# Kernel tuning notes

Measured on AMD Instinct MI355X. Metric: run time of the kernel, lower is better.

Reference implementation:

```python
import jax, jax.numpy as jnp
import numpy as np

GRID_SIZE = 5
SPLINE_ORDER = 3
N_COEF = GRID_SIZE + SPLINE_ORDER  # 8
NUM_NODES = 100000
NUM_EDGES = 1200000
NUM_GRAPHS = 512
D = 64
N_TARGETS = 10


def _grid():
    # uniform grid on [-1, 1] extended by spline_order knots on each side (efficient-kan default)
    h = 2.0 / GRID_SIZE
    return jnp.arange(-SPLINE_ORDER, GRID_SIZE + SPLINE_ORDER + 1, dtype=jnp.float32) * h - 1.0


def b_splines(x):
    # x: (N, in) -> (N, in, N_COEF) via Cox-de Boor recursion
    g = _grid()
    xe = x[..., None]
    bases = ((xe >= g[:-1]) & (xe < g[1:])).astype(x.dtype)
    for k in range(1, SPLINE_ORDER + 1):
        left = (xe - g[: -(k + 1)]) / (g[k:-1] - g[: -(k + 1)])
        right = (g[k + 1:] - xe) / (g[k + 1:] - g[1:-k])
        bases = left * bases[..., :-1] + right * bases[..., 1:]
    return bases


def kan_linear(x, base_w, spline_w, scaler):
    # efficient-kan KANLinear: silu base branch + standalone-scaled spline branch
    base = jax.nn.silu(x) @ base_w.T
    sb = b_splines(x)  # (N, in, N_COEF)
    spline = jnp.einsum('nig,oig->no', sb, spline_w * scaler[..., None])
    return base + spline


def setup_inputs() -> dict:
    key = jax.random.key(0)
    ks = jax.random.split(key, 12)
    inp = {
        'x': jax.random.normal(ks[0], (NUM_NODES, D), dtype=jnp.float32),
        'edge_index': jax.random.randint(ks[1], (2, NUM_EDGES), 0, NUM_NODES, dtype=jnp.int64),
        'batch': jnp.sort(jax.random.randint(ks[2], (NUM_NODES,), 0, NUM_GRAPHS, dtype=jnp.int64)),
        # GINConv layer 0 KAN (D -> D)
        'base_w0': jax.random.normal(ks[3], (D, D), dtype=jnp.float32) * 0.1,
        'spline_w0': jax.random.normal(ks[4], (D, D, N_COEF), dtype=jnp.float32) * 0.1,
        'scaler0': jax.random.normal(ks[5], (D, D), dtype=jnp.float32) * 0.1 + 1.0,
        # GINConv layer 1 KAN (D -> D)
        'base_w1': jax.random.normal(ks[6], (D, D), dtype=jnp.float32) * 0.1,
        'spline_w1': jax.random.normal(ks[7], (D, D, N_COEF), dtype=jnp.float32) * 0.1,
        'scaler1': jax.random.normal(ks[8], (D, D), dtype=jnp.float32) * 0.1 + 1.0,
        # head KAN (D -> N_TARGETS)
        'base_wh': jax.random.normal(ks[9], (N_TARGETS, D), dtype=jnp.float32) * 0.1,
        'spline_wh': jax.random.normal(ks[10], (N_TARGETS, D, N_COEF), dtype=jnp.float32) * 0.1,
        'scaler_h': jax.random.normal(ks[11], (N_TARGETS, D), dtype=jnp.float32) * 0.1 + 1.0,
    }
    return inp


def reference(x, edge_index, batch, base_w0, spline_w0, scaler0,
              base_w1, spline_w1, scaler1, base_wh, spline_wh, scaler_h):
    src, dst = edge_index[0], edge_index[1]
    n = x.shape[0]
    # GINConv layer 0: nn((1+eps)*x + sum_{j in N(i)} x_j), eps=0; dropout is eval-mode identity
    agg = jax.ops.segment_sum(x[src], dst, num_segments=n)
    h = kan_linear(x + agg, base_w0, spline_w0, scaler0)
    # GINConv layer 1
    agg = jax.ops.segment_sum(h[src], dst, num_segments=n)
    h = kan_linear(h + agg, base_w1, spline_w1, scaler1)
    # global_add_pool over graphs, then KAN head
    pooled = jax.ops.segment_sum(h, batch, num_segments=NUM_GRAPHS)
    return kan_linear(pooled, base_wh, spline_wh, scaler_h)
```

## Files before the change

kernel.cpp:

```cpp
#include <hip/hip_runtime.h>
#include <hip/hip_fp16.h>
#include <math.h>

#define NODES   100000
#define EDGES   1200000
#define GRAPHS  512
#define DIM     64
#define NT      10
#define KTOT    576

#define NB      512
#define NBUSED  391
#define EPB     4096
#define CAP     4608

#define KSTAGE     96
#define WTL_STRIDE 104
#define V_STRIDE   72

#define S3B     ((EDGES + EPB - 1) / EPB)
#define PREPB   ((2 * DIM * KTOT) / 512)
#define CONVB   ((NODES * 16 + 32 + 511) / 512)

typedef _Float16 f16x8  __attribute__((ext_vector_type(8)));
typedef __fp16   fp16x2 __attribute__((ext_vector_type(2)));
typedef __attribute__((ext_vector_type(4))) float frag_cd;

__device__ __forceinline__ float silu(float x) {
    return x / (1.f + __expf(-x));
}

__device__ __forceinline__ unsigned packh2(float a, float b) {
    fp16x2 h = __builtin_amdgcn_cvt_pkrtz(a, b);
    return __builtin_bit_cast(unsigned, h);
}

__device__ __forceinline__ void acc_h8(float* a, uint4 p) {
    union { uint4 u; __half2 h[4]; } up; up.u = p;
#pragma unroll
    for (int j = 0; j < 4; ++j) {
        float2 f = __half22float2(up.h[j]);
        a[2 * j]     += f.x;
        a[2 * j + 1] += f.y;
    }
}

__device__ __forceinline__ f16x8 bases_frag(float xv) {
    float tt  = fmaf(xv, 2.5f, 5.5f);
    float fm  = floorf(tt);
    int   m   = (int)fm;
    float u   = tt - fm;
    float um1 = 1.f - u;
    float v3  = u * u * u * (1.f / 6.f);
    float v0  = um1 * um1 * um1 * (1.f / 6.f);
    float B2m1 = 0.5f * ((u + 1.f) * um1 + (2.f - u) * u);
    float v1  = ((u + 2.f) * um1 * um1 * 0.5f + (2.f - u) * B2m1) * (1.f / 3.f);
    float v2  = ((u + 1.f) * B2m1 + (3.f - u) * u * u * 0.5f) * (1.f / 3.f);

    unsigned d0 = packh2(v0, v1);
    unsigned d1 = packh2(v2, v3);
    int p = m - 3;
    int B = p >> 1;
    bool odd = (p & 1) != 0;
    unsigned e1 = __builtin_amdgcn_alignbit(d1, d0, 16);
    unsigned W0 = odd ? (d0 << 16) : d0;
    unsigned W1 = odd ? e1 : d1;
    unsigned W2 = odd ? (d1 >> 16) : 0u;
    union { f16x8 f; unsigned u[4]; } r;
    r.u[0] = (B == 0) ? W0 : ((B == -1) ? W1 : ((B == -2) ? W2 : 0u));
    r.u[1] = (B == 1) ? W0 : ((B ==  0) ? W1 : ((B == -1) ? W2 : 0u));
    r.u[2] = (B == 2) ? W0 : ((B ==  1) ? W1 : ((B ==  0) ? W2 : 0u));
    r.u[3] = (B == 3) ? W0 : ((B ==  2) ? W1 : ((B ==  1) ? W2 : 0u));
    return r.f;
}

__global__ __launch_bounds__(512) void mega(const int* __restrict__ ei,
                                            int* __restrict__ bcur,
                                            unsigned* __restrict__ tmp,
                                            const float* __restrict__ bw0,
                                            const float* __restrict__ sw0,
                                            const float* __restrict__ sc0,
                                            const float* __restrict__ bw1,
                                            const float* __restrict__ sw1,
                                            const float* __restrict__ sc1,
                                            unsigned short* __restrict__ wt0,
                                            unsigned short* __restrict__ wt1,
                                            const float* __restrict__ x,
                                            const int* __restrict__ bat,
                                            unsigned short* __restrict__ xb,
                                            unsigned short* __restrict__ hpad,
                                            int* __restrict__ goff) {
    __shared__ int hist[NB], lstart[NB], gbase[NB], cur[NB];
    __shared__ unsigned ebuf[EPB];
    __shared__ unsigned short bk[EPB];
    const int bx = blockIdx.x;
    const int t  = threadIdx.x;

    if (bx < S3B) {
        hist[t] = 0; cur[t] = 0;
        __syncthreads();
        const int e0 = bx * EPB;
        int src[8], dst[8];
#pragma unroll
        for (int k = 0; k < 8; ++k) {
            int e = e0 + t + k * 512;
            bool valid = e < EDGES;
            src[k] = valid ? ei[e] : 0;
            dst[k] = valid ? ei[EDGES + e] : -1;
            if (valid) atomicAdd(&hist[dst[k] >> 8], 1);
        }
        __syncthreads();
        int v = hist[t];
        lstart[t] = v;
        __syncthreads();
        int run = v;
        for (int d = 1; d < NB; d <<= 1) {
            int a = (t >= d) ? lstart[t - d] : 0;
            __syncthreads();
            run += a; lstart[t] = run;
            __syncthreads();
        }
        lstart[t] = run - v;
        if (v) gbase[t] = atomicAdd(&bcur[t], v);
        __syncthreads();
#pragma unroll
        for (int k = 0; k < 8; ++k) {
            if (dst[k] >= 0) {
                int b = dst[k] >> 8;
                int pos = lstart[b] + atomicAdd(&cur[b], 1);
                ebuf[pos] = (unsigned)src[k] | ((unsigned)(dst[k] & 255) << 24);
                bk[pos] = (unsigned short)b;
            }
        }
        __syncthreads();
        int total = EDGES - e0; if (total > EPB) total = EPB;
        for (int i = t; i < total; i += 512) {
            int b = bk[i];
            tmp[(size_t)b * CAP + gbase[b] + (i - lstart[b])] = ebuf[i];
        }
        return;
    }

    if (bx < S3B + PREPB) {
        int idx = (bx - S3B) * 512 + t;
        int layer = idx >= DIM * KTOT;
        int li = layer ? idx - DIM * KTOT : idx;
        const float* bw = layer ? bw1 : bw0;
        const float* sw = layer ? sw1 : sw0;
        const float* sc = layer ? sc1 : sc0;
        unsigned short* wt = layer ? wt1 : wt0;
        int o = li / KTOT, k = li % KTOT;
        float v;
        if (k < DIM) {
            v = bw[o * DIM + k];
        } else {
            int i = (k - DIM) >> 3, g = (k - DIM) & 7;
            v = sw[(o * DIM + i) * 8 + g] * sc[o * DIM + i];
        }
        wt[li] = __half_as_ushort(__float2half(v));
        return;
    }

    int i = (bx - S3B - PREPB) * 512 + t;
    if (i < NODES * 16) {
        float4 v = ((const float4*)x)[i];
        unsigned lo = packh2(v.x, v.y);
        unsigned hi = packh2(v.z, v.w);
        ((uint2*)xb)[i] = make_uint2(lo, hi);
        if ((i & 15) == 0) {
            int n = i >> 4;
            int b  = bat[n];
            int bp = (n == 0) ? -1 : bat[n - 1];
            for (int g = bp + 1; g <= b; ++g) goff[g] = n;
        }
        if (i == 0) {
            int blast = bat[NODES - 1];
            for (int g = blast + 1; g <= GRAPHS; ++g) goff[g] = NODES;
        }
    } else {
        int j = i - NODES * 16;
        if (j < 16)      ((uint2*)xb)[NODES * 16 + j] = make_uint2(0, 0);
        else if (j < 32) ((uint2*)hpad)[j - 16]       = make_uint2(0, 0);
    }
}

__global__ __launch_bounds__(1024) void s4_fill(const unsigned* __restrict__ tmp,
                                                const int* __restrict__ bcur,
                                                int2* __restrict__ rowp,
                                                int* __restrict__ col) {
    __shared__ int deg[256], scanI[256], cur[256];
    __shared__ int tot;
    __shared__ int4 colbuf4[CAP / 4];
    int* colbuf = (int*)colbuf4;
    const int b = blockIdx.x, t = threadIdx.x;
    const int cnt = bcur[b];
    const int base = b * CAP;
    if (t < 256) deg[t] = 0;
    __syncthreads();
    for (int i = t; i < cnt; i += 1024)
        atomicAdd(&deg[tmp[base + i] >> 24], 1);
    __syncthreads();
    if (t < 256) scanI[t] = (deg[t] + 3) & ~3;
    __syncthreads();
    for (int d = 1; d < 256; d <<= 1) {
        int a = 0;
        if (t < 256 && t >= d) a = scanI[t - d];
        __syncthreads();
        if (t < 256) scanI[t] += a;
        __syncthreads();
    }
    if (t < 256) {
        int pad = (deg[t] + 3) & ~3;
        int start = scanI[t] - pad;
        int ng = b * 256 + t;
        if (ng < NODES) rowp[ng] = make_int2(base + start, base + start + pad);
        cur[t] = start;
        if (t == 255) tot = scanI[255];
    }
    __syncthreads();
    for (int i = t; i < cnt; i += 1024) {
        unsigned p = tmp[base + i];
        int pos = atomicAdd(&cur[p >> 24], 1);
        colbuf[pos] = (int)(p & 0xFFFFFFu);
    }
    __syncthreads();
    if (t < 256) {
        int pad = (deg[t] + 3) & ~3;
        int end = scanI[t] - pad + pad;
        for (int k = cur[t]; k < end; ++k) colbuf[k] = NODES;
    }
    __syncthreads();
    int nq = tot >> 2;
    int4* out4 = (int4*)(col + base);
    for (int i = t; i < nq; i += 1024) out4[i] = colbuf4[i];
}

__global__ __launch_bounds__(256) void fused_layer(const unsigned short* __restrict__ xin,
                                                   const int2* __restrict__ rowp,
                                                   const int* __restrict__ col,
                                                   const unsigned short* __restrict__ wt,
                                                   unsigned short* __restrict__ out) {
    __shared__ unsigned short wt_lds[64 * WTL_STRIDE];
    __shared__ unsigned short v_lds[64 * V_STRIDE];

    const int t     = threadIdx.x;
    const int nbase = blockIdx.x * 64;

    uint4 p0, p1, p2;
    {
        int c0 = t, c1 = t + 256, c2 = t + 512;
        p0 = *(const uint4*)(wt + (c0 / 12) * KTOT + (c0 % 12) * 8);
        p1 = *(const uint4*)(wt + (c1 / 12) * KTOT + (c1 % 12) * 8);
        p2 = *(const uint4*)(wt + (c2 / 12) * KTOT + (c2 % 12) * 8);
    }

    const uint4* x4 = (const uint4*)xin;
#pragma unroll
    for (int rd = 0; rd < 2; ++rd) {
        int idx  = t + rd * 256;
        int node = idx >> 3, c8 = idx & 7;
        int n = nbase + node;
        uint4 res = make_uint4(0, 0, 0, 0);
        if (n < NODES) {
            int2 be = rowp[n];
            float a0[8], a1[8], a2[8], a3[8];
#pragma unroll
            for (int j = 0; j < 8; ++j) { a0[j] = 0.f; a1[j] = 0.f; a2[j] = 0.f; a3[j] = 0.f; }
            acc_h8(a0, x4[n * 8 + c8]);
            for (int p = be.x; p < be.y; p += 4) {
                int4 c4 = *(const int4*)(col + p);
                uint4 r0 = x4[c4.x * 8 + c8];
                uint4 r1 = x4[c4.y * 8 + c8];
                uint4 r2 = x4[c4.z * 8 + c8];
                uint4 r3 = x4[c4.w * 8 + c8];
                acc_h8(a0, r0); acc_h8(a1, r1); acc_h8(a2, r2); acc_h8(a3, r3);
            }
            union { uint4 u; unsigned w[4]; } rr;
#pragma unroll
            for (int j = 0; j < 4; ++j) {
                float lo = a0[2 * j]     + a1[2 * j]     + a2[2 * j]     + a3[2 * j];
                float hi = a0[2 * j + 1] + a1[2 * j + 1] + a2[2 * j + 1] + a3[2 * j + 1];
                rr.w[j] = packh2(lo, hi);
            }
            res = rr.u;
        }
        *(uint4*)(v_lds + node * V_STRIDE + c8 * 8) = res;
    }
    {
        int c0 = t, c1 = t + 256, c2 = t + 512;
        *(uint4*)(wt_lds + (c0 / 12) * WTL_STRIDE + (c0 % 12) * 8) = p0;
        *(uint4*)(wt_lds + (c1 / 12) * WTL_STRIDE + (c1 % 12) * 8) = p1;
        *(uint4*)(wt_lds + (c2 / 12) * WTL_STRIDE + (c2 % 12) * 8) = p2;
    }
    __syncthreads();

    const int w = t >> 6;
    const int l = t & 63;
    const int q = l >> 4;
    const int c = l & 15;
    const unsigned short* vrow = v_lds + ((w << 4) + c) * V_STRIDE;

    frag_cd ac0 = {0.f, 0.f, 0.f, 0.f};
    frag_cd ac1 = {0.f, 0.f, 0.f, 0.f};
    frag_cd ac2 = {0.f, 0.f, 0.f, 0.f};
    frag_cd ac3 = {0.f, 0.f, 0.f, 0.f};

#define MSTEP(OFF, A) {                                                          \
        f16x8 b0 = *(const f16x8*)(wt_lds + (c     ) * WTL_STRIDE + (OFF));      \
        f16x8 b1 = *(const f16x8*)(wt_lds + (c + 16) * WTL_STRIDE + (OFF));      \
        f16x8 b2 = *(const f16x8*)(wt_lds + (c + 32) * WTL_STRIDE + (OFF));      \
        f16x8 b3 = *(const f16x8*)(wt_lds + (c + 48) * WTL_STRIDE + (OFF));      \
        ac0 = __builtin_amdgcn_mfma_f32_16x16x32_f16(A, b0, ac0, 0, 0, 0);       \
        ac1 = __builtin_amdgcn_mfma_f32_16x16x32_f16(A, b1, ac1, 0, 0, 0);       \
        ac2 = __builtin_amdgcn_mfma_f32_16x16x32_f16(A, b2, ac2, 0, 0, 0);       \
        ac3 = __builtin_amdgcn_mfma_f32_16x16x32_f16(A, b3, ac3, 0, 0, 0); }

    {
        int c0 = t, c1 = t + 256, c2 = t + 512;
        p0 = *(const uint4*)(wt + (c0 / 12) * KTOT + KSTAGE + (c0 % 12) * 8);
        p1 = *(const uint4*)(wt + (c1 / 12) * KTOT + KSTAGE + (c1 % 12) * 8);
        p2 = *(const uint4*)(wt + (c2 / 12) * KTOT + KSTAGE + (c2 % 12) * 8);
    }

#pragma unroll
    for (int s = 0; s < 2; ++s) {
        f16x8 hv = *(const f16x8*)(vrow + 32 * s + 8 * q);
        float f[8];
#pragma unroll
        for (int j = 0; j < 8; ++j) f[j] = silu((float)hv[j]);
        union { f16x8 v; unsigned u[4]; } a;
#pragma unroll
        for (int j = 0; j < 4; ++j) a.u[j] = packh2(f[2 * j], f[2 * j + 1]);
        MSTEP(32 * s + 8 * q, a.v);
    }
    {
        f16x8 a = bases_frag((float)(*(const _Float16*)(vrow + q)));
        MSTEP(64 + 8 * q, a);
    }

#pragma unroll
    for (int st = 1; st < 6; ++st) {
        __syncthreads();
        {
            int c0 = t, c1 = t + 256, c2 = t + 512;
            *(uint4*)(wt_lds + (c0 / 12) * WTL_STRIDE + (c0 % 12) * 8) = p0;
            *(uint4*)(wt_lds + (c1 / 12) * WTL_STRIDE + (c1 % 12) * 8) = p1;
            *(uint4*)(wt_lds + (c2 / 12) * WTL_STRIDE + (c2 % 12) * 8) = p2;
        }
        __syncthreads();
        if (st < 5) {
            int c0 = t, c1 = t + 256, c2 = t + 512;
            p0 = *(const uint4*)(wt + (c0 / 12) * KTOT + (st + 1) * KSTAGE + (c0 % 12) * 8);
            p1 = *(const uint4*)(wt + (c1 / 12) * KTOT + (st + 1) * KSTAGE + (c1 % 12) * 8);
            p2 = *(const uint4*)(wt + (c2 / 12) * KTOT + (st + 1) * KSTAGE + (c2 % 12) * 8);
        }
#pragma unroll
        for (int k = 0; k < 3; ++k) {
            int s = 3 * st + k;
            f16x8 a = bases_frag((float)(*(const _Float16*)(vrow + 4 * s + q - 8)));
            MSTEP(32 * k + 8 * q, a);
        }
    }
#undef MSTEP

    const int n0 = nbase + (w << 4) + (q << 2);
#pragma unroll
    for (int r = 0; r < 4; ++r) {
        int n = n0 + r;
        if (n < NODES) {
            unsigned short* o = out + (size_t)n * DIM + c;
            o[0]  = __half_as_ushort(__float2half(ac0[r]));
            o[16] = __half_as_ushort(__float2half(ac1[r]));
            o[32] = __half_as_ushort(__float2half(ac2[r]));
            o[48] = __half_as_ushort(__float2half(ac3[r]));
        }
    }
}

__global__ __launch_bounds__(256) void pool_head(const unsigned short* __restrict__ h,
                                                 const int* __restrict__ goff,
                                                 const float* __restrict__ bwh,
                                                 const float* __restrict__ swh,
                                                 const float* __restrict__ sch,
                                                 float* __restrict__ out) {
    __shared__ float ps[8][64];
    const int g = blockIdx.x, t = threadIdx.x;
    const int start = goff[g], end = goff[g + 1];
    const int d2 = t & 31, grp = t >> 5;
    float s0 = 0.f, s1 = 0.f;
    for (int n = start + grp; n < end; n += 8) {
        __half2 hv = *(const __half2*)(h + (size_t)n * DIM + 2 * d2);
        float2 f = __half22float2(hv);
        s0 += f.x;
        s1 += f.y;
    }
    ps[grp][2 * d2]     = s0;
    ps[grp][2 * d2 + 1] = s1;
    __syncthreads();

    if (t < 64) {
        const int i = t;
        float xv = 0.f;
#pragma unroll
        for (int k = 0; k < 8; ++k) xv += ps[k][i];

        float s  = silu(xv);
        float tt  = fmaf(xv, 2.5f, 5.5f);
        float fm  = floorf(tt);
        int   m   = (int)fm;
        float u   = tt - fm;
        float um1 = 1.f - u;
        float v3  = u * u * u * (1.f / 6.f);
        float v0  = um1 * um1 * um1 * (1.f / 6.f);
        float B2m1 = 0.5f * ((u + 1.f) * um1 + (2.f - u) * u);
        float v1  = ((u + 2.f) * um1 * um1 * 0.5f + (2.f - u) * B2m1) * (1.f / 3.f);
        float v2  = ((u + 1.f) * B2m1 + (3.f - u) * u * u * 0.5f) * (1.f / 3.f);
        bool inr  = (m >= 0) && (m <= 10);
        float b[8];
#pragma unroll
        for (int j = 0; j < 8; ++j) {
            float bv = 0.f;
            bv = (j == m - 3) ? v0 : bv;
            bv = (j == m - 2) ? v1 : bv;
            bv = (j == m - 1) ? v2 : bv;
            bv = (j == m)     ? v3 : bv;
            b[j] = inr ? bv : 0.f;
        }

        float part[NT];
#pragma unroll
        for (int o = 0; o < NT; ++o) {
            const float* sp = swh + (o * DIM + i) * 8;
            float sb = 0.f;
#pragma unroll
            for (int qq = 0; qq < 8; ++qq) sb = fmaf(b[qq], sp[qq], sb);
            part[o] = fmaf(s, bwh[o * DIM + i], sb * sch[o * DIM + i]);
        }
#pragma unroll
        for (int o = 0; o < NT; ++o) {
            float v = part[o];
#pragma unroll
            for (int off = 32; off > 0; off >>= 1) v += __shfl_down(v, off, 64);
            if (i == 0) out[g * NT + o] = v;
        }
    }
}

extern "C" void kernel_launch(void* const* d_in, const int* in_sizes, int n_in,
                              void* d_out, int out_size, void* d_ws, size_t ws_size,
                              hipStream_t stream) {
    const float* x   = (const float*)d_in[0];
    const int*   ei  = (const int*)d_in[1];
    const int*   bat = (const int*)d_in[2];
    const float* bw0 = (const float*)d_in[3];
    const float* sw0 = (const float*)d_in[4];
    const float* sc0 = (const float*)d_in[5];
    const float* bw1 = (const float*)d_in[6];
    const float* sw1 = (const float*)d_in[7];
    const float* sc1 = (const float*)d_in[8];
    const float* bwh = (const float*)d_in[9];
    const float* swh = (const float*)d_in[10];
    const float* sch = (const float*)d_in[11];
    float* out = (float*)d_out;

    const size_t ROW = (size_t)(NODES + 1) * DIM;

    unsigned short* wt0 = (unsigned short*)d_ws;
    unsigned short* wt1 = wt0 + DIM * KTOT;
    unsigned short* xbf = wt1 + DIM * KTOT;
    unsigned short* hbf = xbf + ROW;
    unsigned short* h2  = hbf + ROW;
    int* goff     = (int*)(h2 + (size_t)NODES * DIM);
    int2* rowp    = (int2*)(goff + 514);
    int* col      = (int*)(rowp + NODES);
    int* bcur     = col + (size_t)NB * CAP;
    unsigned* tmp = (unsigned*)(bcur + NB);

    (void)hipMemsetAsync(bcur, 0, NB * sizeof(int), stream);

    mega<<<S3B + PREPB + CONVB, 512, 0, stream>>>(
        ei, bcur, tmp,
        bw0, sw0, sc0, bw1, sw1, sc1, wt0, wt1,
        x, bat, xbf, hbf + (size_t)NODES * DIM, goff);

    s4_fill<<<NBUSED, 1024, 0, stream>>>(tmp, bcur, rowp, col);

    const int layer_blocks = (NODES + 63) / 64;
    fused_layer<<<layer_blocks, 256, 0, stream>>>(xbf, rowp, col, wt0, hbf);
    fused_layer<<<layer_blocks, 256, 0, stream>>>(hbf, rowp, col, wt1, h2);

    pool_head<<<GRAPHS, 256, 0, stream>>>(h2, goff, bwh, swh, sch, out);
}
```

Before: 214.5 us.

## Shrink weight staging, accumulate gathers in half2, simplify spline polynomials

Cuts the K-stage from 96 to 64 with a smaller LDS stride and raises launch bounds to 8 blocks per CU, so occupancy can go up at the cost of more stages and barriers. Neighbor aggregation now accumulates directly in packed half2 instead of fp32, which removes conversions but loses accumulation precision. Spline basis evaluation uses Horner/fma polynomial forms, and silu uses a hardware reciprocal approximation instead of a divide. Together these aim to lower ALU and register pressure in the fused layer.

```diff
diff --git a/kernel.cpp b/kernel.cpp
--- a/kernel.cpp
+++ b/kernel.cpp
@@ -14,8 +14,8 @@
 #define EPB     4096
 #define CAP     4608
 
-#define KSTAGE     96
-#define WTL_STRIDE 104
+#define KSTAGE     64
+#define WTL_STRIDE 72
 #define V_STRIDE   72
 
 #define S3B     ((EDGES + EPB - 1) / EPB)
@@ -27,7 +27,7 @@
 typedef __attribute__((ext_vector_type(4))) float frag_cd;
 
 __device__ __forceinline__ float silu(float x) {
-    return x / (1.f + __expf(-x));
+    return x * __builtin_amdgcn_rcpf(1.f + __expf(-x));
 }
 
 __device__ __forceinline__ unsigned packh2(float a, float b) {
@@ -35,27 +35,19 @@
     return __builtin_bit_cast(unsigned, h);
 }
 
-__device__ __forceinline__ void acc_h8(float* a, uint4 p) {
-    union { uint4 u; __half2 h[4]; } up; up.u = p;
-#pragma unroll
-    for (int j = 0; j < 4; ++j) {
-        float2 f = __half22float2(up.h[j]);
-        a[2 * j]     += f.x;
-        a[2 * j + 1] += f.y;
-    }
-}
+union H8 { uint4 u; __half2 h[4]; };
 
 __device__ __forceinline__ f16x8 bases_frag(float xv) {
     float tt  = fmaf(xv, 2.5f, 5.5f);
     float fm  = floorf(tt);
     int   m   = (int)fm;
     float u   = tt - fm;
-    float um1 = 1.f - u;
-    float v3  = u * u * u * (1.f / 6.f);
-    float v0  = um1 * um1 * um1 * (1.f / 6.f);
-    float B2m1 = 0.5f * ((u + 1.f) * um1 + (2.f - u) * u);
-    float v1  = ((u + 2.f) * um1 * um1 * 0.5f + (2.f - u) * B2m1) * (1.f / 3.f);
-    float v2  = ((u + 1.f) * B2m1 + (3.f - u) * u * u * 0.5f) * (1.f / 3.f);
+    float u2  = u * u;
+    float u3  = u2 * u;
+    float v0  = fmaf(fmaf(fmaf(u, -(1.f / 6.f), 0.5f), u, -0.5f), u, 1.f / 6.f);
+    float v1  = fmaf(u3, 0.5f, fmaf(u2, -1.f, 2.f / 3.f));
+    float v2  = fmaf(u + u2 - u3, 0.5f, 1.f / 6.f);
+    float v3  = u3 * (1.f / 6.f);
 
     unsigned d0 = packh2(v0, v1);
     unsigned d1 = packh2(v2, v3);
@@ -235,23 +227,22 @@
     for (int i = t; i < nq; i += 1024) out4[i] = colbuf4[i];
 }
 
-__global__ __launch_bounds__(256) void fused_layer(const unsigned short* __restrict__ xin,
-                                                   const int2* __restrict__ rowp,
-                                                   const int* __restrict__ col,
-                                                   const unsigned short* __restrict__ wt,
-                                                   unsigned short* __restrict__ out) {
+__global__ __launch_bounds__(256, 8) void fused_layer(const unsigned short* __restrict__ xin,
+                                                      const int2* __restrict__ rowp,
+                                                      const int* __restrict__ col,
+                                                      const unsigned short* __restrict__ wt,
+                                                      unsigned short* __restrict__ out) {
     __shared__ unsigned short wt_lds[64 * WTL_STRIDE];
     __shared__ unsigned short v_lds[64 * V_STRIDE];
 
     const int t     = threadIdx.x;
     const int nbase = blockIdx.x * 64;
 
-    uint4 p0, p1, p2;
+    uint4 p0, p1;
     {
-        int c0 = t, c1 = t + 256, c2 = t + 512;
-        p0 = *(const uint4*)(wt + (c0 / 12) * KTOT + (c0 % 12) * 8);
-        p1 = *(const uint4*)(wt + (c1 / 12) * KTOT + (c1 % 12) * 8);
-        p2 = *(const uint4*)(wt + (c2 / 12) * KTOT + (c2 % 12) * 8);
+        int c0 = t, c1 = t + 256;
+        p0 = *(const uint4*)(wt + (c0 >> 3) * KTOT + (c0 & 7) * 8);
+        p1 = *(const uint4*)(wt + (c1 >> 3) * KTOT + (c1 & 7) * 8);
     }
 
     const uint4* x4 = (const uint4*)xin;
@@ -263,34 +254,37 @@
         uint4 res = make_uint4(0, 0, 0, 0);
         if (n < NODES) {
             int2 be = rowp[n];
-            float a0[8], a1[8], a2[8], a3[8];
-#pragma unroll
-            for (int j = 0; j < 8; ++j) { a0[j] = 0.f; a1[j] = 0.f; a2[j] = 0.f; a3[j] = 0.f; }
-            acc_h8(a0, x4[n * 8 + c8]);
+            H8 a0, a1, a2, a3;
+            a0.u = x4[n * 8 + c8];
+            a1.u = make_uint4(0, 0, 0, 0);
+            a2.u = make_uint4(0, 0, 0, 0);
+            a3.u = make_uint4(0, 0, 0, 0);
             for (int p = be.x; p < be.y; p += 4) {
                 int4 c4 = *(const int4*)(col + p);
-                uint4 r0 = x4[c4.x * 8 + c8];
-                uint4 r1 = x4[c4.y * 8 + c8];
-                uint4 r2 = x4[c4.z * 8 + c8];
-                uint4 r3 = x4[c4.w * 8 + c8];
-                acc_h8(a0, r0); acc_h8(a1, r1); acc_h8(a2, r2); acc_h8(a3, r3);
+                H8 r0, r1, r2, r3;
+                r0.u = x4[c4.x * 8 + c8];
+                r1.u = x4[c4.y * 8 + c8];
+                r2.u = x4[c4.z * 8 + c8];
+                r3.u = x4[c4.w * 8 + c8];
+#pragma unroll
+                for (int j = 0; j < 4; ++j) {
+                    a0.h[j] = __hadd2(a0.h[j], r0.h[j]);
+                    a1.h[j] = __hadd2(a1.h[j], r1.h[j]);
+                    a2.h[j] = __hadd2(a2.h[j], r2.h[j]);
+                    a3.h[j] = __hadd2(a3.h[j], r3.h[j]);
+                }
             }
-            union { uint4 u; unsigned w[4]; } rr;
-#pragma unroll
-            for (int j = 0; j < 4; ++j) {
-                float lo = a0[2 * j]     + a1[2 * j]     + a2[2 * j]     + a3[2 * j];
-                float hi = a0[2 * j + 1] + a1[2 * j + 1] + a2[2 * j + 1] + a3[2 * j + 1];
-                rr.w[j] = packh2(lo, hi);
-            }
-            res = rr.u;
+#pragma unroll
+            for (int j = 0; j < 4; ++j)
+                a0.h[j] = __hadd2(__hadd2(a0.h[j], a1.h[j]), __hadd2(a2.h[j], a3.h[j]));
+            res = a0.u;
         }
         *(uint4*)(v_lds + node * V_STRIDE + c8 * 8) = res;
     }
     {
-        int c0 = t, c1 = t + 256, c2 = t + 512;
-        *(uint4*)(wt_lds + (c0 / 12) * WTL_STRIDE + (c0 % 12) * 8) = p0;
-        *(uint4*)(wt_lds + (c1 / 12) * WTL_STRIDE + (c1 % 12) * 8) = p1;
-        *(uint4*)(wt_lds + (c2 / 12) * WTL_STRIDE + (c2 % 12) * 8) = p2;
+        int c0 = t, c1 = t + 256;
+        *(uint4*)(wt_lds + (c0 >> 3) * WTL_STRIDE + (c0 & 7) * 8) = p0;
+        *(uint4*)(wt_lds + (c1 >> 3) * WTL_STRIDE + (c1 & 7) * 8) = p1;
     }
     __syncthreads();
 
@@ -316,10 +310,9 @@
         ac3 = __builtin_amdgcn_mfma_f32_16x16x32_f16(A, b3, ac3, 0, 0, 0); }
 
     {
-        int c0 = t, c1 = t + 256, c2 = t + 512;
-        p0 = *(const uint4*)(wt + (c0 / 12) * KTOT + KSTAGE + (c0 % 12) * 8);
-        p1 = *(const uint4*)(wt + (c1 / 12) * KTOT + KSTAGE + (c1 % 12) * 8);
-        p2 = *(const uint4*)(wt + (c2 / 12) * KTOT + KSTAGE + (c2 % 12) * 8);
+        int c0 = t, c1 = t + 256;
+        p0 = *(const uint4*)(wt + (c0 >> 3) * KTOT + KSTAGE + (c0 & 7) * 8);
+        p1 = *(const uint4*)(wt + (c1 >> 3) * KTOT + KSTAGE + (c1 & 7) * 8);
     }
 
 #pragma unroll
@@ -333,32 +326,25 @@
         for (int j = 0; j < 4; ++j) a.u[j] = packh2(f[2 * j], f[2 * j + 1]);
         MSTEP(32 * s + 8 * q, a.v);
     }
-    {
-        f16x8 a = bases_frag((float)(*(const _Float16*)(vrow + q)));
-        MSTEP(64 + 8 * q, a);
-    }
-
-#pragma unroll
-    for (int st = 1; st < 6; ++st) {
+
+#pragma unroll
+    for (int st = 1; st < 9; ++st) {
         __syncthreads();
         {
-            int c0 = t, c1 = t + 256, c2 = t + 512;
-            *(uint4*)(wt_lds + (c0 / 12) * WTL_STRIDE + (c0 % 12) * 8) = p0;
-            *(uint4*)(wt_lds + (c1 / 12) * WTL_STRIDE + (c1 % 12) * 8) = p1;
-            *(uint4*)(wt_lds + (c2 / 12) * WTL_STRIDE + (c2 % 12) * 8) = p2;
-        }
-        __syncthreads();
-        if (st < 5) {
-            int c0 = t, c1 = t + 256, c2 = t + 512;
-            p0 = *(const uint4*)(wt + (c0 / 12) * KTOT + (st + 1) * KSTAGE + (c0 % 12) * 8);
-            p1 = *(const uint4*)(wt + (c1 / 12) * KTOT + (st + 1) * KSTAGE + (c1 % 12) * 8);
-            p2 = *(const uint4*)(wt + (c2 / 12) * KTOT + (st + 1) * KSTAGE + (c2 % 12) * 8);
-        }
-#pragma unroll
-        for (int k = 0; k < 3; ++k) {
-            int s = 3 * st + k;
-            f16x8 a = bases_frag((float)(*(const _Float16*)(vrow + 4 * s + q - 8)));
-            MSTEP(32 * k + 8 * q, a);
+            int c0 = t, c1 = t + 256;
+            *(uint4*)(wt_lds + (c0 >> 3) * WTL_STRIDE + (c0 & 7) * 8) = p0;
+            *(uint4*)(wt_lds + (c1 >> 3) * WTL_STRIDE + (c1 & 7) * 8) = p1;
+        }
+        __syncthreads();
+        if (st < 8) {
+            int c0 = t, c1 = t + 256;
+            p0 = *(const uint4*)(wt + (c0 >> 3) * KTOT + (st + 1) * KSTAGE + (c0 & 7) * 8);
+            p1 = *(const uint4*)(wt + (c1 >> 3) * KTOT + (st + 1) * KSTAGE + (c1 & 7) * 8);
+        }
+#pragma unroll
+        for (int k2 = 0; k2 < 2; ++k2) {
+            f16x8 a = bases_frag((float)(*(const _Float16*)(vrow + 8 * (st - 1) + 4 * k2 + q)));
+            MSTEP(32 * k2 + 8 * q, a);
         }
     }
 #undef MSTEP
@@ -409,12 +395,12 @@
         float fm  = floorf(tt);
         int   m   = (int)fm;
         float u   = tt - fm;
-        float um1 = 1.f - u;
-        float v3  = u * u * u * (1.f / 6.f);
-        float v0  = um1 * um1 * um1 * (1.f / 6.f);
-        float B2m1 = 0.5f * ((u + 1.f) * um1 + (2.f - u) * u);
-        float v1  = ((u + 2.f) * um1 * um1 * 0.5f + (2.f - u) * B2m1) * (1.f / 3.f);
-        float v2  = ((u + 1.f) * B2m1 + (3.f - u) * u * u * 0.5f) * (1.f / 3.f);
+        float u2  = u * u;
+        float u3  = u2 * u;
+        float v0  = fmaf(fmaf(fmaf(u, -(1.f / 6.f), 0.5f), u, -0.5f), u, 1.f / 6.f);
+        float v1  = fmaf(u3, 0.5f, fmaf(u2, -1.f, 2.f / 3.f));
+        float v2  = fmaf(u + u2 - u3, 0.5f, 1.f / 6.f);
+        float v3  = u3 * (1.f / 6.f);
         bool inr  = (m >= 0) && (m <= 10);
         float b[8];
 #pragma unroll
```

After: 200.9 us. 6.4% less time.
